# Kernel tuning notes

Measured on AMD Instinct MI355X. Metric: run time of the kernel, lower is better.

Reference implementation:

```python
import jax, jax.numpy as jnp
import numpy as np

HIDDEN = 1024
NUM_HEADS = 16
HEAD_DIM = HIDDEN // NUM_HEADS
B, S = 4, 4096


def setup_inputs() -> dict:
    key = jax.random.key(0)
    ks = jax.random.split(key, 7)
    scale = 1.0 / np.sqrt(HIDDEN)
    return {
        "hidden_states": jax.random.normal(ks[0], (B, S, HIDDEN), dtype=jnp.float32),
        "Wq": jax.random.normal(ks[1], (HIDDEN, HIDDEN), dtype=jnp.float32) * scale,
        "bq": jax.random.normal(ks[2], (HIDDEN,), dtype=jnp.float32) * 0.01,
        "Wk": jax.random.normal(ks[3], (HIDDEN, HIDDEN), dtype=jnp.float32) * scale,
        "bk": jax.random.normal(ks[4], (HIDDEN,), dtype=jnp.float32) * 0.01,
        "Wv": jax.random.normal(ks[5], (HIDDEN, HIDDEN), dtype=jnp.float32) * scale,
        "bv": jax.random.normal(ks[6], (HIDDEN,), dtype=jnp.float32) * 0.01,
    }


def _split_heads(x):
    # [B, S, H*D] -> [B, H, S, D]
    b, s, _ = x.shape
    return x.reshape(b, s, NUM_HEADS, HEAD_DIM).transpose(0, 2, 1, 3)


def reference(hidden_states, Wq, bq, Wk, bk, Wv, bv):
    # Fused-style QKV: single stacked GEMM, then split + reshape to heads.
    Wqkv = jnp.concatenate([Wq, Wk, Wv], axis=1)          # [H, 3H]
    bqkv = jnp.concatenate([bq, bk, bv], axis=0)           # [3H]
    qkv = jnp.einsum("bsh,hf->bsf", hidden_states, Wqkv) + bqkv  # [B, S, 3H]
    q, k, v = jnp.split(qkv, 3, axis=-1)
    return (_split_heads(q), _split_heads(k), _split_heads(v))
```

## Files before the change

### kernel.cpp

```cpp
#include <hip/hip_runtime.h>
#include <hip/hip_bf16.h>


#define M_TOT 16384
#define N_TOT 3072
#define K_TOT 1024

typedef __bf16 bf16x8 __attribute__((ext_vector_type(8)));
typedef float f32x16 __attribute__((ext_vector_type(16)));

#define AS1(p) ((const __attribute__((address_space(1))) void*)(p))
#define AS3(p) ((__attribute__((address_space(3))) void*)(p))

__device__ __forceinline__ unsigned short f2bf(float f) {
    unsigned int u = __builtin_bit_cast(unsigned int, f);
    u += 0x7fffu + ((u >> 16) & 1u);
    return (unsigned short)(u >> 16);
}

__global__ void convert_hidden(const float* __restrict__ x,
                               unsigned short* __restrict__ y, int n4) {
    int i = blockIdx.x * blockDim.x + threadIdx.x;
    int stride = gridDim.x * blockDim.x;
    for (; i < n4; i += stride) {
        float4 v = ((const float4*)x)[i];
        ushort4 o;
        o.x = f2bf(v.x); o.y = f2bf(v.y); o.z = f2bf(v.z); o.w = f2bf(v.w);
        ((ushort4*)y)[i] = o;
    }
}

__global__ void convert_weights(const float* __restrict__ Wq,
                                const float* __restrict__ Wk,
                                const float* __restrict__ Wv,
                                unsigned short* __restrict__ Bt) {
    __shared__ unsigned short tile[64][65];
    const float* W = (blockIdx.z == 0) ? Wq : (blockIdx.z == 1) ? Wk : Wv;
    int k0 = blockIdx.y * 64;
    int f0 = blockIdx.x * 64;
    int tx = threadIdx.x & 63;
    int ty = threadIdx.x >> 6;
#pragma unroll
    for (int r = 0; r < 16; ++r) {
        int k = ty + r * 4;
        tile[k][tx] = f2bf(W[(size_t)(k0 + k) * 1024 + f0 + tx]);
    }
    __syncthreads();
#pragma unroll
    for (int r = 0; r < 16; ++r) {
        int fr = ty + r * 4;
        Bt[(size_t)(blockIdx.z * 1024 + f0 + fr) * 1024 + k0 + tx] = tile[tx][fr];
    }
}

__launch_bounds__(256, 2)
__global__ void qkv_gemm(const unsigned short* __restrict__ A,
                         const unsigned short* __restrict__ Bt,
                         const float* __restrict__ bq,
                         const float* __restrict__ bk,
                         const float* __restrict__ bv,
                         float* __restrict__ out) {
    __shared__ __align__(16) unsigned short As[128 * 32];
    __shared__ __align__(16) unsigned short Bs[128 * 32];

    const int tid  = threadIdx.x;
    const int wave = tid >> 6;
    const int lane = tid & 63;
    const int r5   = lane & 31;
    const int half = lane >> 5;

    const int bm = blockIdx.x;
    const int bn = blockIdx.y;

    const int wr = wave >> 1;
    const int wc = wave & 1;

    f32x16 acc[2][2] = {};

    const int c0 = wave * 64 + lane;
    const int rowA0 = c0 >> 2;
    const int k8A0  = ((c0 & 3) ^ ((rowA0 >> 1) & 3)) * 8;
    const int c1 = 256 + c0;
    const int rowA1 = c1 >> 2;
    const int k8A1  = ((c1 & 3) ^ ((rowA1 >> 1) & 3)) * 8;

    const unsigned short* gA0 = A  + (size_t)(bm * 128 + rowA0) * 1024 + k8A0;
    const unsigned short* gA1 = A  + (size_t)(bm * 128 + rowA1) * 1024 + k8A1;
    const unsigned short* gB0 = Bt + (size_t)(bn * 128 + rowA0) * 1024 + k8A0;
    const unsigned short* gB1 = Bt + (size_t)(bn * 128 + rowA1) * 1024 + k8A1;

    unsigned short* ldsA0 = As + (size_t)(wave)*512;
    unsigned short* ldsA1 = As + (size_t)(4 + wave) * 512;
    unsigned short* ldsB0 = Bs + (size_t)(wave)*512;
    unsigned short* ldsB1 = Bs + (size_t)(4 + wave) * 512;

    const int swsel = (r5 >> 1) & 3;

    for (int k0 = 0; k0 < K_TOT; k0 += 32) {
        __builtin_amdgcn_global_load_lds(AS1(gA0 + k0), AS3(ldsA0), 16, 0, 0);
        __builtin_amdgcn_global_load_lds(AS1(gA1 + k0), AS3(ldsA1), 16, 0, 0);
        __builtin_amdgcn_global_load_lds(AS1(gB0 + k0), AS3(ldsB0), 16, 0, 0);
        __builtin_amdgcn_global_load_lds(AS1(gB1 + k0), AS3(ldsB1), 16, 0, 0);
        __syncthreads();

        bf16x8 av[2][2], bvv[2][2];
#pragma unroll
        for (int ib = 0; ib < 2; ++ib) {
            int arow = wr * 64 + ib * 32 + r5;
#pragma unroll
            for (int ks = 0; ks < 2; ++ks) {
                int p = (ks * 2 + half) ^ swsel;
                av[ib][ks] = *(const bf16x8*)&As[arow * 32 + p * 8];
            }
        }
#pragma unroll
        for (int jb = 0; jb < 2; ++jb) {
            int brow = wc * 64 + jb * 32 + r5;
#pragma unroll
            for (int ks = 0; ks < 2; ++ks) {
                int p = (ks * 2 + half) ^ swsel;
                bvv[jb][ks] = *(const bf16x8*)&Bs[brow * 32 + p * 8];
            }
        }
#pragma unroll
        for (int ks = 0; ks < 2; ++ks)
#pragma unroll
            for (int ib = 0; ib < 2; ++ib)
#pragma unroll
                for (int jb = 0; jb < 2; ++jb)
                    acc[ib][jb] = __builtin_amdgcn_mfma_f32_32x32x16_bf16(
                        av[ib][ks], bvv[jb][ks], acc[ib][jb], 0, 0, 0);
        __syncthreads();
    }

    const int section = (bn * 128) >> 10;
    const int nloc0   = (bn * 128 - section * 1024) + wc * 64;
    const float* bias = (section == 0) ? bq : (section == 1) ? bk : bv;
    float* outsec = out + (size_t)section * (4u * 16u * 4096u * 64u);

#pragma unroll
    for (int jb = 0; jb < 2; ++jb) {
        int f = nloc0 + jb * 32 + r5;
        float bval = bias[f];
        int h = f >> 6, d = f & 63;
        size_t hb = (size_t)h * (4096u * 64u);
#pragma unroll
        for (int ib = 0; ib < 2; ++ib) {
            int mbase = bm * 128 + wr * 64 + ib * 32 + 4 * half;
#pragma unroll
            for (int reg = 0; reg < 16; ++reg) {
                int m = mbase + (reg & 3) + 8 * (reg >> 2);
                int b = m >> 12, s = m & 4095;
                outsec[(size_t)b * (16u * 4096u * 64u) + hb + (size_t)s * 64u + d] =
                    acc[ib][jb][reg] + bval;
            }
        }
    }
}

extern "C" void kernel_launch(void* const* d_in, const int* in_sizes, int n_in,
                              void* d_out, int out_size, void* d_ws, size_t ws_size,
                              hipStream_t stream) {
    const float* hs = (const float*)d_in[0];
    const float* Wq = (const float*)d_in[1];
    const float* bq = (const float*)d_in[2];
    const float* Wk = (const float*)d_in[3];
    const float* bk = (const float*)d_in[4];
    const float* Wv = (const float*)d_in[5];
    const float* bv = (const float*)d_in[6];
    float* out = (float*)d_out;

    unsigned short* Abf  = (unsigned short*)d_ws;
    unsigned short* Btbf = Abf + (size_t)M_TOT * K_TOT;

    convert_hidden<<<2048, 256, 0, stream>>>(hs, Abf, (M_TOT * K_TOT) / 4);
    convert_weights<<<dim3(16, 16, 3), 256, 0, stream>>>(Wq, Wk, Wv, Btbf);
    qkv_gemm<<<dim3(M_TOT / 128, N_TOT / 128), 256, 0, stream>>>(Abf, Btbf, bq, bk, bv, out);
}
```

Measured before the change: 371.6 us.

## Pre-tile operands into MFMA fragment layout and drop LDS staging in GEMM

The conversion kernels now write A and B in a panel layout where each wave's MFMA fragment for one k-step is a contiguous 1KB block. The GEMM then loads fragments straight from global memory into registers with a two-deep register prefetch, removing shared memory and the per-iteration barriers. Occupancy is raised to three blocks per SM. The trade-off is that each wave now reads its operands from global or L2 on its own, without any sharing across the block through LDS, which raises global traffic per block. Load latency is also covered only by a shallow prefetch.

Result: slower. 400.1 us (+7.7%).

```diff
diff --git a/kernel.cpp b/kernel.cpp
--- a/kernel.cpp
+++ b/kernel.cpp
@@ -7,10 +7,8 @@
 #define K_TOT 1024
 
 typedef __bf16 bf16x8 __attribute__((ext_vector_type(8)));
+typedef unsigned short ushx8 __attribute__((ext_vector_type(8)));
 typedef float f32x16 __attribute__((ext_vector_type(16)));
-
-#define AS1(p) ((const __attribute__((address_space(1))) void*)(p))
-#define AS3(p) ((__attribute__((address_space(3))) void*)(p))
 
 __device__ __forceinline__ unsigned short f2bf(float f) {
     unsigned int u = __builtin_bit_cast(unsigned int, f);
@@ -19,14 +17,21 @@
 }
 
 __global__ void convert_hidden(const float* __restrict__ x,
-                               unsigned short* __restrict__ y, int n4) {
-    int i = blockIdx.x * blockDim.x + threadIdx.x;
-    int stride = gridDim.x * blockDim.x;
-    for (; i < n4; i += stride) {
-        float4 v = ((const float4*)x)[i];
-        ushort4 o;
-        o.x = f2bf(v.x); o.y = f2bf(v.y); o.z = f2bf(v.z); o.w = f2bf(v.w);
-        ((ushort4*)y)[i] = o;
+                               unsigned short* __restrict__ At) {
+    const int panel = blockIdx.x;
+    const int t = threadIdx.x;
+    const int wave = t >> 6, lane = t & 63;
+    const int r5 = lane & 31, half = lane >> 5;
+    const float* src = x + (size_t)(panel * 32 + r5) * 1024 + half * 8;
+    unsigned short* dst = At + (size_t)panel * 32768 + lane * 8;
+#pragma unroll 4
+    for (int ks = wave * 16; ks < wave * 16 + 16; ++ks) {
+        float4 f0 = *(const float4*)(src + ks * 16);
+        float4 f1 = *(const float4*)(src + ks * 16 + 4);
+        ushx8 o;
+        o[0] = f2bf(f0.x); o[1] = f2bf(f0.y); o[2] = f2bf(f0.z); o[3] = f2bf(f0.w);
+        o[4] = f2bf(f1.x); o[5] = f2bf(f1.y); o[6] = f2bf(f1.z); o[7] = f2bf(f1.w);
+        *(ushx8*)(dst + ks * 512) = o;
     }
 }
 
@@ -34,35 +39,32 @@
                                 const float* __restrict__ Wk,
                                 const float* __restrict__ Wv,
                                 unsigned short* __restrict__ Bt) {
-    __shared__ unsigned short tile[64][65];
-    const float* W = (blockIdx.z == 0) ? Wq : (blockIdx.z == 1) ? Wk : Wv;
-    int k0 = blockIdx.y * 64;
-    int f0 = blockIdx.x * 64;
-    int tx = threadIdx.x & 63;
-    int ty = threadIdx.x >> 6;
+    const int panel = blockIdx.x;
+    const int mat = panel >> 5;
+    const int n0 = (panel & 31) * 32;
+    const float* W = (mat == 0) ? Wq : (mat == 1) ? Wk : Wv;
+    const int t = threadIdx.x;
+    const int wave = t >> 6, lane = t & 63;
+    const int r5 = lane & 31, half = lane >> 5;
+    const float* src = W + (size_t)half * 8 * 1024 + n0 + r5;
+    unsigned short* dst = Bt + (size_t)panel * 32768 + lane * 8;
+#pragma unroll 2
+    for (int ks = wave * 16; ks < wave * 16 + 16; ++ks) {
+        ushx8 o;
 #pragma unroll
-    for (int r = 0; r < 16; ++r) {
-        int k = ty + r * 4;
-        tile[k][tx] = f2bf(W[(size_t)(k0 + k) * 1024 + f0 + tx]);
-    }
-    __syncthreads();
-#pragma unroll
-    for (int r = 0; r < 16; ++r) {
-        int fr = ty + r * 4;
-        Bt[(size_t)(blockIdx.z * 1024 + f0 + fr) * 1024 + k0 + tx] = tile[tx][fr];
+        for (int j = 0; j < 8; ++j)
+            o[j] = f2bf(src[(size_t)(ks * 16 + j) * 1024]);
+        *(ushx8*)(dst + ks * 512) = o;
     }
 }
 
-__launch_bounds__(256, 2)
-__global__ void qkv_gemm(const unsigned short* __restrict__ A,
+__launch_bounds__(256, 3)
+__global__ void qkv_gemm(const unsigned short* __restrict__ At,
                          const unsigned short* __restrict__ Bt,
                          const float* __restrict__ bq,
                          const float* __restrict__ bk,
                          const float* __restrict__ bv,
                          float* __restrict__ out) {
-    __shared__ __align__(16) unsigned short As[128 * 32];
-    __shared__ __align__(16) unsigned short Bs[128 * 32];
-
     const int tid  = threadIdx.x;
     const int wave = tid >> 6;
     const int lane = tid & 63;
@@ -71,66 +73,39 @@
 
     const int bm = blockIdx.x;
     const int bn = blockIdx.y;
-
     const int wr = wave >> 1;
     const int wc = wave & 1;
 
+    const unsigned short* pa0 = At + (size_t)(bm * 4 + wr * 2 + 0) * 32768 + lane * 8;
+    const unsigned short* pa1 = At + (size_t)(bm * 4 + wr * 2 + 1) * 32768 + lane * 8;
+    const unsigned short* pb0 = Bt + (size_t)(bn * 4 + wc * 2 + 0) * 32768 + lane * 8;
+    const unsigned short* pb1 = Bt + (size_t)(bn * 4 + wc * 2 + 1) * 32768 + lane * 8;
+
     f32x16 acc[2][2] = {};
 
-    const int c0 = wave * 64 + lane;
-    const int rowA0 = c0 >> 2;
-    const int k8A0  = ((c0 & 3) ^ ((rowA0 >> 1) & 3)) * 8;
-    const int c1 = 256 + c0;
-    const int rowA1 = c1 >> 2;
-    const int k8A1  = ((c1 & 3) ^ ((rowA1 >> 1) & 3)) * 8;
+    bf16x8 a0[2], a1[2], b0[2], b1[2];
+#pragma unroll
+    for (int p = 0; p < 2; ++p) {
+        a0[p] = *(const bf16x8*)(pa0 + p * 512);
+        a1[p] = *(const bf16x8*)(pa1 + p * 512);
+        b0[p] = *(const bf16x8*)(pb0 + p * 512);
+        b1[p] = *(const bf16x8*)(pb1 + p * 512);
+    }
 
-    const unsigned short* gA0 = A  + (size_t)(bm * 128 + rowA0) * 1024 + k8A0;
-    const unsigned short* gA1 = A  + (size_t)(bm * 128 + rowA1) * 1024 + k8A1;
-    const unsigned short* gB0 = Bt + (size_t)(bn * 128 + rowA0) * 1024 + k8A0;
-    const unsigned short* gB1 = Bt + (size_t)(bn * 128 + rowA1) * 1024 + k8A1;
-
-    unsigned short* ldsA0 = As + (size_t)(wave)*512;
-    unsigned short* ldsA1 = As + (size_t)(4 + wave) * 512;
-    unsigned short* ldsB0 = Bs + (size_t)(wave)*512;
-    unsigned short* ldsB1 = Bs + (size_t)(4 + wave) * 512;
-
-    const int swsel = (r5 >> 1) & 3;
-
-    for (int k0 = 0; k0 < K_TOT; k0 += 32) {
-        __builtin_amdgcn_global_load_lds(AS1(gA0 + k0), AS3(ldsA0), 16, 0, 0);
-        __builtin_amdgcn_global_load_lds(AS1(gA1 + k0), AS3(ldsA1), 16, 0, 0);
-        __builtin_amdgcn_global_load_lds(AS1(gB0 + k0), AS3(ldsB0), 16, 0, 0);
-        __builtin_amdgcn_global_load_lds(AS1(gB1 + k0), AS3(ldsB1), 16, 0, 0);
-        __syncthreads();
-
-        bf16x8 av[2][2], bvv[2][2];
 #pragma unroll
-        for (int ib = 0; ib < 2; ++ib) {
-            int arow = wr * 64 + ib * 32 + r5;
-#pragma unroll
-            for (int ks = 0; ks < 2; ++ks) {
-                int p = (ks * 2 + half) ^ swsel;
-                av[ib][ks] = *(const bf16x8*)&As[arow * 32 + p * 8];
-            }
+    for (int ks = 0; ks < 64; ++ks) {
+        const int slot = ks & 1;
+        bf16x8 ca0 = a0[slot], ca1 = a1[slot], cb0 = b0[slot], cb1 = b1[slot];
+        if (ks + 2 < 64) {
+            a0[slot] = *(const bf16x8*)(pa0 + (ks + 2) * 512);
+            a1[slot] = *(const bf16x8*)(pa1 + (ks + 2) * 512);
+            b0[slot] = *(const bf16x8*)(pb0 + (ks + 2) * 512);
+            b1[slot] = *(const bf16x8*)(pb1 + (ks + 2) * 512);
         }
-#pragma unroll
-        for (int jb = 0; jb < 2; ++jb) {
-            int brow = wc * 64 + jb * 32 + r5;
-#pragma unroll
-            for (int ks = 0; ks < 2; ++ks) {
-                int p = (ks * 2 + half) ^ swsel;
-                bvv[jb][ks] = *(const bf16x8*)&Bs[brow * 32 + p * 8];
-            }
-        }
-#pragma unroll
-        for (int ks = 0; ks < 2; ++ks)
-#pragma unroll
-            for (int ib = 0; ib < 2; ++ib)
-#pragma unroll
-                for (int jb = 0; jb < 2; ++jb)
-                    acc[ib][jb] = __builtin_amdgcn_mfma_f32_32x32x16_bf16(
-                        av[ib][ks], bvv[jb][ks], acc[ib][jb], 0, 0, 0);
-        __syncthreads();
+        acc[0][0] = __builtin_amdgcn_mfma_f32_32x32x16_bf16(ca0, cb0, acc[0][0], 0, 0, 0);
+        acc[0][1] = __builtin_amdgcn_mfma_f32_32x32x16_bf16(ca0, cb1, acc[0][1], 0, 0, 0);
+        acc[1][0] = __builtin_amdgcn_mfma_f32_32x32x16_bf16(ca1, cb0, acc[1][0], 0, 0, 0);
+        acc[1][1] = __builtin_amdgcn_mfma_f32_32x32x16_bf16(ca1, cb1, acc[1][1], 0, 0, 0);
     }
 
     const int section = (bn * 128) >> 10;
@@ -170,10 +145,10 @@
     const float* bv = (const float*)d_in[6];
     float* out = (float*)d_out;
 
-    unsigned short* Abf  = (unsigned short*)d_ws;
-    unsigned short* Btbf = Abf + (size_t)M_TOT * K_TOT;
+    unsigned short* Atld = (unsigned short*)d_ws;
+    unsigned short* Btld = Atld + (size_t)M_TOT * K_TOT;
 
-    convert_hidden<<<2048, 256, 0, stream>>>(hs, Abf, (M_TOT * K_TOT) / 4);
-    convert_weights<<<dim3(16, 16, 3), 256, 0, stream>>>(Wq, Wk, Wv, Btbf);
-    qkv_gemm<<<dim3(M_TOT / 128, N_TOT / 128), 256, 0, stream>>>(Abf, Btbf, bq, bk, bv, out);
+    convert_hidden<<<512, 256, 0, stream>>>(hs, Atld);
+    convert_weights<<<96, 256, 0, stream>>>(Wq, Wk, Wv, Btld);
+    qkv_gemm<<<dim3(M_TOT / 128, N_TOT / 128), 256, 0, stream>>>(Atld, Btld, bq, bk, bv, out);
 }
```
